# Optimization experiments

Measured on AMD Instinct MI355X. Metric: run time of the kernel, lower is better.

## Reference

```python
import jax, jax.numpy as jnp
import numpy as np

B, S, N, H = 16, 512, 64, 768
E_TYPES, R_TYPES = 9, 10


def setup_inputs() -> dict:
    key = jax.random.key(0)
    ks = jax.random.split(key, 8)
    seq = jax.random.normal(ks[0], (B, S, H), dtype=jnp.float32)
    starts = jax.random.randint(ks[1], (B, N), 0, S - 16)
    lengths = jax.random.randint(ks[2], (B, N), 1, 16)
    entity_spans = jnp.stack([starts, starts + lengths], axis=-1).astype(jnp.int32)  # [B,N,2], start<end<=S
    attention_mask = jnp.ones((B, S), dtype=jnp.int32)
    sc = 0.02
    return {
        "sequence_output": seq,
        "attention_mask": attention_mask,
        "entity_spans": entity_spans,
        "W1e": jax.random.normal(ks[3], (H, H // 2), dtype=jnp.float32) * sc,
        "b1e": jnp.zeros((H // 2,), dtype=jnp.float32),
        "W2e": jax.random.normal(ks[4], (H // 2, E_TYPES), dtype=jnp.float32) * sc,
        "b2e": jnp.zeros((E_TYPES,), dtype=jnp.float32),
        "W1r": jax.random.normal(ks[5], (2 * H, H), dtype=jnp.float32) * sc,
        "b1r": jnp.zeros((H,), dtype=jnp.float32),
        "W2r": jax.random.normal(ks[6], (H, R_TYPES), dtype=jnp.float32) * sc,
        "b2r": jnp.zeros((R_TYPES,), dtype=jnp.float32),
    }


def reference(sequence_output, attention_mask, entity_spans,
              W1e, b1e, W2e, b2e, W1r, b1r, W2r, b2r):
    # Entity classifier over all tokens (dropout = identity in eval mode).
    # entity_logits: [B, S, E_TYPES]
    entity_logits = jax.nn.relu(sequence_output @ W1e + b1e) @ W2e + b2e

    # Span-mean entity representations, vectorized (replaces the Python
    # per-entity loop with .item() syncs). span mask: [B, N, S]
    pos = jnp.arange(S, dtype=entity_spans.dtype)
    start = entity_spans[..., 0:1]
    end = entity_spans[..., 1:2]
    span_mask = ((pos >= start) & (pos < end)).astype(sequence_output.dtype)
    counts = jnp.maximum(span_mask.sum(-1, keepdims=True), 1.0)
    # entity_repr: [B, N, H] = mean over tokens in each span
    entity_repr = jnp.einsum('bns,bsh->bnh', span_mask, sequence_output) / counts

    # Relation classification for all ordered pairs i<j (replaces nested
    # per-pair micro-launches with one batched GEMM).
    ii, jj = jnp.triu_indices(N, k=1)  # static, P = N*(N-1)/2
    pair_repr = jnp.concatenate([entity_repr[:, ii, :], entity_repr[:, jj, :]], axis=-1)  # [B,P,2H]
    relation_logits = jax.nn.relu(pair_repr @ W1r + b1r) @ W2r + b2r  # [B,P,R_TYPES]

    return entity_logits, entity_repr, relation_logits
```

## Files before the change

### kernel.cpp

```cpp
#include <hip/hip_runtime.h>
#include <hip/hip_bf16.h>


#define S_LEN 512
#define H_DIM 768
#define NPAIR 2016

typedef __bf16 bf16x8 __attribute__((ext_vector_type(8)));
typedef float f32x4 __attribute__((ext_vector_type(4)));

__device__ __forceinline__ void gload_lds16(const void* g, void* l) {
    __builtin_amdgcn_global_load_lds(
        (const __attribute__((address_space(1))) void*)g,
        (__attribute__((address_space(3))) void*)l, 16, 0, 0);
}

__device__ __forceinline__ ushort f2bf(float x) {
    __hip_bfloat16 h = __float2bfloat16(x);
    return *(ushort*)&h;
}

__global__ __launch_bounds__(256) void prep_all_k(
    const float* __restrict__ seq, const int* __restrict__ spans,
    const float* __restrict__ W1e, const float* __restrict__ W1r,
    const float* __restrict__ W2e, const float* __restrict__ W2r,
    const float* __restrict__ b2r,
    float* __restrict__ erep, ushort* __restrict__ erep_bf,
    ushort* __restrict__ W1et, ushort* __restrict__ W1rt,
    ushort* __restrict__ W2et, ushort* __restrict__ W2rt,
    int* __restrict__ ptab, float* __restrict__ rlog,
    ushort* __restrict__ seq_bf)
{
    __shared__ float t[32][33];
    const int bid = blockIdx.x, tid = threadIdx.x;

    if (bid < 1024) {
        const int bn = bid, b = bn >> 6;
        const int s0 = spans[bn * 2], s1 = spans[bn * 2 + 1];
        int lo = s0 < 0 ? 0 : s0;
        int hi = s1 > S_LEN ? S_LEN : s1;
        int cnt = hi - lo;
        if (cnt < 1) cnt = 1;
        const float inv = 1.f / (float)cnt;
        for (int c = tid; c < H_DIM; c += 256) {
            float acc = 0.f;
            for (int s = lo; s < hi; ++s)
                acc += seq[((size_t)b * S_LEN + s) * H_DIM + c];
            float v = acc * inv;
            erep[(size_t)bn * H_DIM + c] = v;
            erep_bf[(size_t)bn * H_DIM + c] = f2bf(v);
        }
    } else if (bid < 2464) {
        const float* src; ushort* dst; int b2, C;
        if (bid < 1312)      { b2 = bid - 1024; src = W1e; dst = W1et; C = 384; }
        else if (bid < 1888) { b2 = bid - 1312; src = W1r; dst = W1rt; C = 768; }
        else                 { b2 = bid - 1888; src = W1r + 768 * 768; dst = W1rt + 768 * 768; C = 768; }
        const int br = b2 % 24, bc = b2 / 24;
        const int r = tid >> 5, c = tid & 31;
        #pragma unroll
        for (int p = 0; p < 4; ++p) {
            int rr = r + p * 8;
            t[rr][c] = src[(size_t)(br * 32 + rr) * C + bc * 32 + c];
        }
        __syncthreads();
        #pragma unroll
        for (int p = 0; p < 4; ++p) {
            int rr = r + p * 8;
            dst[(size_t)(bc * 32 + rr) * 768 + br * 32 + c] = f2bf(t[c][rr]);
        }
    } else if (bid < 2552) {
        int idx = (bid - 2464) * 256 + tid;
        if (idx < 12288) {
            int col = idx / 768, k = idx % 768;
            W2rt[idx] = (col < 10) ? f2bf(W2r[k * 10 + col]) : (ushort)0;
        } else if (idx < 18432) {
            int u = idx - 12288;
            int col = u / 384, k = u % 384;
            W2et[u] = (col < 9) ? f2bf(W2e[k * 9 + col]) : (ushort)0;
        } else {
            int u = idx - 18432;
            int i = u >> 6, j = u & 63;
            if (j > i) {
                int p = i * 63 - i * (i - 1) / 2 + (j - i - 1);
                ptab[p] = (i << 8) | j;
            }
        }
    } else if (bid < 2680) {
        for (int n = (bid - 2552) * 256 + tid; n < 16 * NPAIR * 10; n += 128 * 256)
            rlog[n] = b2r[n % 10];
    } else {
        for (int i = (bid - 2680) * 256 + tid; i < (8192 * 768) / 4; i += 1024 * 256) {
            float4 v = ((const float4*)seq)[i];
            ushort4 o;
            o.x = f2bf(v.x); o.y = f2bf(v.y); o.z = f2bf(v.z); o.w = f2bf(v.w);
            ((ushort4*)seq_bf)[i] = o;
        }
    }
}

template<int EPI>
__device__ __forceinline__ void gemm_body(
    const ushort* __restrict__ A, const ushort* __restrict__ Bt,
    const float* __restrict__ bias, void* __restrict__ Cout,
    int bx, int by, int N, int K, ushort* As, ushort* Bs)
{
    const int tid = threadIdx.x;
    const int lane = tid & 63, wid = tid >> 6;
    const int wr = wid >> 1, wc = wid & 1;
    const int m0 = by * 64, n0 = bx * 128;
    const int fr = lane & 15, kg = lane >> 4;

    const int srow = tid >> 2, skq = (tid & 3) * 8;
    const ushort* ag0 = A + (size_t)(m0 + srow) * K + skq;
    const ushort* bg0 = Bt + (size_t)(n0 + srow) * K + skq;
    const ushort* bg1 = Bt + (size_t)(n0 + 64 + srow) * K + skq;

    int aoff[2], boff[4];
    #pragma unroll
    for (int i = 0; i < 2; ++i)
        aoff[i] = (wr * 32 + i * 16 + fr) * 32 + kg * 8;
    #pragma unroll
    for (int i = 0; i < 4; ++i)
        boff[i] = (wc * 64 + i * 16 + fr) * 32 + kg * 8;

    const int nsteps = K / 32;

    auto STAGE = [&](int kt, int buf) {
        const int kn = kt * 32;
        gload_lds16(ag0 + kn, As + buf * 2048 + tid * 8);
        gload_lds16(bg0 + kn, Bs + buf * 4096 + tid * 8);
        gload_lds16(bg1 + kn, Bs + buf * 4096 + 2048 + tid * 8);
    };

    STAGE(0, 0);
    STAGE(1, 1);
    STAGE(2, 2);

    f32x4 acc[2][4] = {};

    for (int t = 0; t < nsteps; ++t) {
        if (t < nsteps - 2)       asm volatile("s_waitcnt vmcnt(6)" ::: "memory");
        else if (t == nsteps - 2) asm volatile("s_waitcnt vmcnt(3)" ::: "memory");
        else                      asm volatile("s_waitcnt vmcnt(0)" ::: "memory");
        __builtin_amdgcn_s_barrier();
        __builtin_amdgcn_sched_barrier(0);
        if (t + 3 < nsteps) STAGE(t + 3, (t + 3) & 3);
        const int buf = t & 3;
        bf16x8 af[2], bv[4];
        #pragma unroll
        for (int i = 0; i < 2; ++i) af[i] = *(const bf16x8*)&As[buf * 2048 + aoff[i]];
        #pragma unroll
        for (int i = 0; i < 4; ++i) bv[i] = *(const bf16x8*)&Bs[buf * 4096 + boff[i]];
        #pragma unroll
        for (int mi = 0; mi < 2; ++mi)
            #pragma unroll
            for (int nj = 0; nj < 4; ++nj)
                acc[mi][nj] = __builtin_amdgcn_mfma_f32_16x16x32_bf16(
                    af[mi], bv[nj], acc[mi][nj], 0, 0, 0);
    }

    if (EPI == 0) {
        __hip_bfloat16* Cb = (__hip_bfloat16*)Cout;
        float bcol[4];
        #pragma unroll
        for (int nj = 0; nj < 4; ++nj) bcol[nj] = bias[n0 + wc * 64 + nj * 16 + fr];
        #pragma unroll
        for (int mi = 0; mi < 2; ++mi)
            #pragma unroll
            for (int j = 0; j < 4; ++j) {
                size_t rb = (size_t)(m0 + wr * 32 + mi * 16 + kg * 4 + j) * N
                          + n0 + wc * 64 + fr;
                #pragma unroll
                for (int nj = 0; nj < 4; ++nj)
                    Cb[rb + nj * 16] = __float2bfloat16(
                        fmaxf(acc[mi][nj][j] + bcol[nj], 0.f));
            }
    } else {
        float* Cf = (float*)Cout;
        #pragma unroll
        for (int mi = 0; mi < 2; ++mi)
            #pragma unroll
            for (int j = 0; j < 4; ++j) {
                size_t rb = (size_t)(m0 + wr * 32 + mi * 16 + kg * 4 + j) * N
                          + n0 + wc * 64 + fr;
                #pragma unroll
                for (int nj = 0; nj < 4; ++nj)
                    Cf[rb + nj * 16] = acc[mi][nj][j];
            }
    }
}

__global__ __launch_bounds__(256) void gemm2_k(
    const ushort* __restrict__ seq_bf, const ushort* __restrict__ W1et,
    const float* __restrict__ b1e, ushort* __restrict__ H1bf,
    const ushort* __restrict__ erep_bf, const ushort* __restrict__ W1rt,
    float* __restrict__ UV)
{
    __shared__ ushort As[4 * 2048];
    __shared__ ushort Bs[4 * 4096];
    const int bid = blockIdx.x;
    if (bid < 384) {
        gemm_body<0>(seq_bf, W1et, b1e, H1bf, bid % 3, bid / 3, 384, 768, As, Bs);
    } else {
        const int b2 = bid - 384;
        gemm_body<1>(erep_bf, W1rt, nullptr, UV, b2 % 12, b2 / 12, 1536, 768, As, Bs);
    }
}

__global__ __launch_bounds__(256) void post_k(
    const float* __restrict__ UV, const float* __restrict__ b1r,
    const ushort* __restrict__ W2rt, const int* __restrict__ ptab,
    float* __restrict__ rlog,
    const ushort* __restrict__ H1, const ushort* __restrict__ W2et,
    const float* __restrict__ b2e, float* __restrict__ elog)
{
    const int tid = threadIdx.x;
    const int lane = tid & 63, wid = tid >> 6;
    const int fr = lane & 15, kg = lane >> 4;
    const int bid = blockIdx.x;

    if (bid < 378) {
        const int pb = bid % 126, kb = bid / 126;
        const int p0 = pb * 256;

        size_t uoff[4], voff[4];
        #pragma unroll
        for (int q = 0; q < 4; ++q) {
            int p = p0 + wid * 64 + q * 16 + fr;
            unsigned bb = (unsigned)p / 2016u;
            unsigned pp = (unsigned)p - bb * 2016u;
            int ij = ptab[pp];
            uoff[q] = ((size_t)(bb * 64 + (ij >> 8))) * 1536;
            voff[q] = ((size_t)(bb * 64 + (ij & 255))) * 1536 + 768;
        }

        f32x4 acc[4] = {};

        for (int c = kb * 8; c < kb * 8 + 8; ++c) {
            const int k0 = c * 32, kk = k0 + kg * 8;
            const bf16x8 bv = *(const bf16x8*)(W2rt + fr * 768 + kk);
            const float4 bb0 = *(const float4*)(b1r + kk);
            const float4 bb1 = *(const float4*)(b1r + kk + 4);
            #pragma unroll
            for (int q = 0; q < 4; ++q) {
                float4 u0 = *(const float4*)(UV + uoff[q] + kk);
                float4 u1 = *(const float4*)(UV + uoff[q] + kk + 4);
                float4 v0 = *(const float4*)(UV + voff[q] + kk);
                float4 v1 = *(const float4*)(UV + voff[q] + kk + 4);
                ushort h[8];
                h[0] = f2bf(fmaxf(u0.x + v0.x + bb0.x, 0.f));
                h[1] = f2bf(fmaxf(u0.y + v0.y + bb0.y, 0.f));
                h[2] = f2bf(fmaxf(u0.z + v0.z + bb0.z, 0.f));
                h[3] = f2bf(fmaxf(u0.w + v0.w + bb0.w, 0.f));
                h[4] = f2bf(fmaxf(u1.x + v1.x + bb1.x, 0.f));
                h[5] = f2bf(fmaxf(u1.y + v1.y + bb1.y, 0.f));
                h[6] = f2bf(fmaxf(u1.z + v1.z + bb1.z, 0.f));
                h[7] = f2bf(fmaxf(u1.w + v1.w + bb1.w, 0.f));
                bf16x8 av = *(bf16x8*)h;
                acc[q] = __builtin_amdgcn_mfma_f32_16x16x32_bf16(av, bv, acc[q], 0, 0, 0);
            }
        }

        if (fr < 10) {
            #pragma unroll
            for (int q = 0; q < 4; ++q)
                #pragma unroll
                for (int j = 0; j < 4; ++j) {
                    int p = p0 + wid * 64 + q * 16 + kg * 4 + j;
                    atomicAdd(&rlog[(size_t)p * 10 + fr], acc[q][j]);
                }
        }
    } else {
        const int rbase = (bid - 378) * 64 + wid * 16;
        f32x4 acc = {};
        #pragma unroll
        for (int c = 0; c < 12; ++c) {
            const int kk = c * 32 + kg * 8;
            bf16x8 av = *(const bf16x8*)(H1 + (size_t)(rbase + fr) * 384 + kk);
            bf16x8 bv = *(const bf16x8*)(W2et + fr * 384 + kk);
            acc = __builtin_amdgcn_mfma_f32_16x16x32_bf16(av, bv, acc, 0, 0, 0);
        }
        if (fr < 9) {
            const float bias = b2e[fr];
            #pragma unroll
            for (int j = 0; j < 4; ++j)
                elog[(size_t)(rbase + kg * 4 + j) * 9 + fr] = acc[j] + bias;
        }
    }
}

extern "C" void kernel_launch(void* const* d_in, const int* in_sizes, int n_in,
                              void* d_out, int out_size, void* d_ws, size_t ws_size,
                              hipStream_t stream)
{
    const float* seq   = (const float*)d_in[0];
    const int*   spans = (const int*)d_in[2];
    const float* W1e   = (const float*)d_in[3];
    const float* b1e   = (const float*)d_in[4];
    const float* W2e   = (const float*)d_in[5];
    const float* b2e   = (const float*)d_in[6];
    const float* W1r   = (const float*)d_in[7];
    const float* b1r   = (const float*)d_in[8];
    const float* W2r   = (const float*)d_in[9];
    const float* b2r   = (const float*)d_in[10];

    float* out  = (float*)d_out;
    float* elog = out;
    float* erep = out + 73728;
    float* rlog = out + 73728 + 786432;

    char* ws = (char*)d_ws;
    ushort* seq_bf  = (ushort*)ws;
    ushort* W1et    = (ushort*)(ws + 12582912);
    ushort* W1rt    = (ushort*)(ws + 13172736);
    ushort* erep_bf = (ushort*)(ws + 15532032);
    ushort* H1bf    = (ushort*)(ws + 17104896);
    ushort* W2rt    = (ushort*)(ws + 23396352);
    int*    ptab    = (int*)   (ws + 23420928);
    ushort* W2et    = (ushort*)(ws + 23428992);
    float*  UV      = (float*) (ws + 23441280);

    prep_all_k<<<3704, 256, 0, stream>>>(seq, spans, W1e, W1r, W2e, W2r, b2r,
                                         erep, erep_bf, W1et, W1rt, W2et, W2rt,
                                         ptab, rlog, seq_bf);
    gemm2_k<<<576, 256, 0, stream>>>(seq_bf, W1et, b1e, H1bf, erep_bf, W1rt, UV);
    post_k<<<506, 256, 0, stream>>>(UV, b1r, W2rt, ptab, rlog,
                                    H1bf, W2et, b2e, elog);
}
```

Before: 150.4 us.

## Tile relation head by entity-pair blocks with bf16 UV and direct stores

```diff
diff --git a/kernel.cpp b/kernel.cpp
--- a/kernel.cpp
+++ b/kernel.cpp
@@ -20,16 +20,25 @@
     return *(ushort*)&h;
 }
 
+__device__ __forceinline__ void bf8_to_f32(const ushort* p, float* f) {
+    const uint* u = (const uint*)p;
+    #pragma unroll
+    for (int i = 0; i < 4; ++i) {
+        uint x = u[i];
+        f[2 * i]     = __uint_as_float(x << 16);
+        f[2 * i + 1] = __uint_as_float(x & 0xffff0000u);
+    }
+}
+
 __global__ __launch_bounds__(256) void prep_all_k(
     const float* __restrict__ seq, const int* __restrict__ spans,
     const float* __restrict__ W1e, const float* __restrict__ W1r,
     const float* __restrict__ W2e, const float* __restrict__ W2r,
-    const float* __restrict__ b2r,
+    const float* __restrict__ b1r,
     float* __restrict__ erep, ushort* __restrict__ erep_bf,
     ushort* __restrict__ W1et, ushort* __restrict__ W1rt,
     ushort* __restrict__ W2et, ushort* __restrict__ W2rt,
-    int* __restrict__ ptab, float* __restrict__ rlog,
-    ushort* __restrict__ seq_bf)
+    float* __restrict__ b1r_ext, ushort* __restrict__ seq_bf)
 {
     __shared__ float t[32][33];
     const int bid = blockIdx.x, tid = threadIdx.x;
@@ -68,7 +77,7 @@
             int rr = r + p * 8;
             dst[(size_t)(bc * 32 + rr) * 768 + br * 32 + c] = f2bf(t[c][rr]);
         }
-    } else if (bid < 2552) {
+    } else if (bid < 2542) {
         int idx = (bid - 2464) * 256 + tid;
         if (idx < 12288) {
             int col = idx / 768, k = idx % 768;
@@ -79,17 +88,10 @@
             W2et[u] = (col < 9) ? f2bf(W2e[k * 9 + col]) : (ushort)0;
         } else {
             int u = idx - 18432;
-            int i = u >> 6, j = u & 63;
-            if (j > i) {
-                int p = i * 63 - i * (i - 1) / 2 + (j - i - 1);
-                ptab[p] = (i << 8) | j;
-            }
-        }
-    } else if (bid < 2680) {
-        for (int n = (bid - 2552) * 256 + tid; n < 16 * NPAIR * 10; n += 128 * 256)
-            rlog[n] = b2r[n % 10];
+            b1r_ext[u] = (u < 768) ? b1r[u] : 0.f;
+        }
     } else {
-        for (int i = (bid - 2680) * 256 + tid; i < (8192 * 768) / 4; i += 1024 * 256) {
+        for (int i = (bid - 2542) * 256 + tid; i < (8192 * 768) / 4; i += 1024 * 256) {
             float4 v = ((const float4*)seq)[i];
             ushort4 o;
             o.x = f2bf(v.x); o.y = f2bf(v.y); o.z = f2bf(v.z); o.w = f2bf(v.w);
@@ -159,42 +161,30 @@
                     af[mi], bv[nj], acc[mi][nj], 0, 0, 0);
     }
 
-    if (EPI == 0) {
-        __hip_bfloat16* Cb = (__hip_bfloat16*)Cout;
-        float bcol[4];
-        #pragma unroll
-        for (int nj = 0; nj < 4; ++nj) bcol[nj] = bias[n0 + wc * 64 + nj * 16 + fr];
-        #pragma unroll
-        for (int mi = 0; mi < 2; ++mi)
-            #pragma unroll
-            for (int j = 0; j < 4; ++j) {
-                size_t rb = (size_t)(m0 + wr * 32 + mi * 16 + kg * 4 + j) * N
-                          + n0 + wc * 64 + fr;
-                #pragma unroll
-                for (int nj = 0; nj < 4; ++nj)
-                    Cb[rb + nj * 16] = __float2bfloat16(
-                        fmaxf(acc[mi][nj][j] + bcol[nj], 0.f));
+    __hip_bfloat16* Cb = (__hip_bfloat16*)Cout;
+    float bcol[4];
+    #pragma unroll
+    for (int nj = 0; nj < 4; ++nj) bcol[nj] = bias[n0 + wc * 64 + nj * 16 + fr];
+    #pragma unroll
+    for (int mi = 0; mi < 2; ++mi)
+        #pragma unroll
+        for (int j = 0; j < 4; ++j) {
+            size_t rb = (size_t)(m0 + wr * 32 + mi * 16 + kg * 4 + j) * N
+                      + n0 + wc * 64 + fr;
+            #pragma unroll
+            for (int nj = 0; nj < 4; ++nj) {
+                float v = acc[mi][nj][j] + bcol[nj];
+                if (EPI == 0) v = fmaxf(v, 0.f);
+                Cb[rb + nj * 16] = __float2bfloat16(v);
             }
-    } else {
-        float* Cf = (float*)Cout;
-        #pragma unroll
-        for (int mi = 0; mi < 2; ++mi)
-            #pragma unroll
-            for (int j = 0; j < 4; ++j) {
-                size_t rb = (size_t)(m0 + wr * 32 + mi * 16 + kg * 4 + j) * N
-                          + n0 + wc * 64 + fr;
-                #pragma unroll
-                for (int nj = 0; nj < 4; ++nj)
-                    Cf[rb + nj * 16] = acc[mi][nj][j];
-            }
-    }
+        }
 }
 
 __global__ __launch_bounds__(256) void gemm2_k(
     const ushort* __restrict__ seq_bf, const ushort* __restrict__ W1et,
     const float* __restrict__ b1e, ushort* __restrict__ H1bf,
     const ushort* __restrict__ erep_bf, const ushort* __restrict__ W1rt,
-    float* __restrict__ UV)
+    const float* __restrict__ b1r_ext, ushort* __restrict__ UVbf)
 {
     __shared__ ushort As[4 * 2048];
     __shared__ ushort Bs[4 * 4096];
@@ -203,14 +193,13 @@
         gemm_body<0>(seq_bf, W1et, b1e, H1bf, bid % 3, bid / 3, 384, 768, As, Bs);
     } else {
         const int b2 = bid - 384;
-        gemm_body<1>(erep_bf, W1rt, nullptr, UV, b2 % 12, b2 / 12, 1536, 768, As, Bs);
+        gemm_body<2>(erep_bf, W1rt, b1r_ext, UVbf, b2 % 12, b2 / 12, 1536, 768, As, Bs);
     }
 }
 
 __global__ __launch_bounds__(256) void post_k(
-    const float* __restrict__ UV, const float* __restrict__ b1r,
-    const ushort* __restrict__ W2rt, const int* __restrict__ ptab,
-    float* __restrict__ rlog,
+    const ushort* __restrict__ UVbf, const ushort* __restrict__ W2rt,
+    const float* __restrict__ b2r, float* __restrict__ rlog,
     const ushort* __restrict__ H1, const ushort* __restrict__ W2et,
     const float* __restrict__ b2e, float* __restrict__ elog)
 {
@@ -219,59 +208,54 @@
     const int fr = lane & 15, kg = lane >> 4;
     const int bid = blockIdx.x;
 
-    if (bid < 378) {
-        const int pb = bid % 126, kb = bid / 126;
-        const int p0 = pb * 256;
-
-        size_t uoff[4], voff[4];
-        #pragma unroll
-        for (int q = 0; q < 4; ++q) {
-            int p = p0 + wid * 64 + q * 16 + fr;
-            unsigned bb = (unsigned)p / 2016u;
-            unsigned pp = (unsigned)p - bb * 2016u;
-            int ij = ptab[pp];
-            uoff[q] = ((size_t)(bb * 64 + (ij >> 8))) * 1536;
-            voff[q] = ((size_t)(bb * 64 + (ij & 255))) * 1536 + 768;
-        }
+    if (bid < 160) {
+        const int t = bid % 10, b = bid / 10;
+        int it, jt;
+        if (t < 4)      { it = 0; jt = t; }
+        else if (t < 7) { it = 1; jt = t - 3; }
+        else if (t < 9) { it = 2; jt = t - 5; }
+        else            { it = 3; jt = 3; }
+        const int i0 = it * 16, j0 = jt * 16;
+        const ushort* Ub = UVbf + (size_t)(b * 64 + i0) * 1536;
+        const ushort* Vb = UVbf + (size_t)(b * 64 + j0) * 1536 + 768;
 
         f32x4 acc[4] = {};
 
-        for (int c = kb * 8; c < kb * 8 + 8; ++c) {
-            const int k0 = c * 32, kk = k0 + kg * 8;
+        for (int c = 0; c < 24; ++c) {
+            const int kk = c * 32 + kg * 8;
             const bf16x8 bv = *(const bf16x8*)(W2rt + fr * 768 + kk);
-            const float4 bb0 = *(const float4*)(b1r + kk);
-            const float4 bb1 = *(const float4*)(b1r + kk + 4);
+            float fv[8];
+            bf8_to_f32(Vb + (size_t)fr * 1536 + kk, fv);
             #pragma unroll
             for (int q = 0; q < 4; ++q) {
-                float4 u0 = *(const float4*)(UV + uoff[q] + kk);
-                float4 u1 = *(const float4*)(UV + uoff[q] + kk + 4);
-                float4 v0 = *(const float4*)(UV + voff[q] + kk);
-                float4 v1 = *(const float4*)(UV + voff[q] + kk + 4);
+                float fu[8];
+                bf8_to_f32(Ub + (size_t)(wid * 4 + q) * 1536 + kk, fu);
                 ushort h[8];
-                h[0] = f2bf(fmaxf(u0.x + v0.x + bb0.x, 0.f));
-                h[1] = f2bf(fmaxf(u0.y + v0.y + bb0.y, 0.f));
-                h[2] = f2bf(fmaxf(u0.z + v0.z + bb0.z, 0.f));
-                h[3] = f2bf(fmaxf(u0.w + v0.w + bb0.w, 0.f));
-                h[4] = f2bf(fmaxf(u1.x + v1.x + bb1.x, 0.f));
-                h[5] = f2bf(fmaxf(u1.y + v1.y + bb1.y, 0.f));
-                h[6] = f2bf(fmaxf(u1.z + v1.z + bb1.z, 0.f));
-                h[7] = f2bf(fmaxf(u1.w + v1.w + bb1.w, 0.f));
+                #pragma unroll
+                for (int e = 0; e < 8; ++e)
+                    h[e] = f2bf(fmaxf(fu[e] + fv[e], 0.f));
                 bf16x8 av = *(bf16x8*)h;
                 acc[q] = __builtin_amdgcn_mfma_f32_16x16x32_bf16(av, bv, acc[q], 0, 0, 0);
             }
         }
 
         if (fr < 10) {
-            #pragma unroll
-            for (int q = 0; q < 4; ++q)
+            const float bias = b2r[fr];
+            #pragma unroll
+            for (int q = 0; q < 4; ++q) {
+                const int i = i0 + wid * 4 + q;
                 #pragma unroll
-                for (int j = 0; j < 4; ++j) {
-                    int p = p0 + wid * 64 + q * 16 + kg * 4 + j;
-                    atomicAdd(&rlog[(size_t)p * 10 + fr], acc[q][j]);
+                for (int jr = 0; jr < 4; ++jr) {
+                    const int j = j0 + kg * 4 + jr;
+                    if (j > i) {
+                        int p = i * 63 - i * (i - 1) / 2 + (j - i - 1);
+                        rlog[((size_t)(b * NPAIR + p)) * 10 + fr] = acc[q][jr] + bias;
+                    }
                 }
+            }
         }
     } else {
-        const int rbase = (bid - 378) * 64 + wid * 16;
+        const int rbase = (bid - 160) * 64 + wid * 16;
         f32x4 acc = {};
         #pragma unroll
         for (int c = 0; c < 12; ++c) {
@@ -316,14 +300,15 @@
     ushort* erep_bf = (ushort*)(ws + 15532032);
     ushort* H1bf    = (ushort*)(ws + 17104896);
     ushort* W2rt    = (ushort*)(ws + 23396352);
-    int*    ptab    = (int*)   (ws + 23420928);
-    ushort* W2et    = (ushort*)(ws + 23428992);
-    float*  UV      = (float*) (ws + 23441280);
-
-    prep_all_k<<<3704, 256, 0, stream>>>(seq, spans, W1e, W1r, W2e, W2r, b2r,
+    ushort* W2et    = (ushort*)(ws + 23420928);
+    float*  b1r_ext = (float*) (ws + 23433216);
+    ushort* UVbf    = (ushort*)(ws + 23439360);
+
+    prep_all_k<<<3566, 256, 0, stream>>>(seq, spans, W1e, W1r, W2e, W2r, b1r,
                                          erep, erep_bf, W1et, W1rt, W2et, W2rt,
-                                         ptab, rlog, seq_bf);
-    gemm2_k<<<576, 256, 0, stream>>>(seq_bf, W1et, b1e, H1bf, erep_bf, W1rt, UV);
-    post_k<<<506, 256, 0, stream>>>(UV, b1r, W2rt, ptab, rlog,
+                                         b1r_ext, seq_bf);
+    gemm2_k<<<576, 256, 0, stream>>>(seq_bf, W1et, b1e, H1bf,
+                                     erep_bf, W1rt, b1r_ext, UVbf);
+    post_k<<<288, 256, 0, stream>>>(UVbf, W2rt, b2r, rlog,
                                     H1bf, W2et, b2e, elog);
 }
```

New measurement: 141.3 us. 1.06x faster.
